# Kernel tuning notes

Hardware: AMD Instinct MI355X
Metric: run time of the kernel (lower is better)

Reference implementation:

```python
import jax, jax.numpy as jnp
import numpy as np

B, T, INP, OUT, H = 64, 512, 256, 256, 512


def _uniform(key, shape, scale):
    return jax.random.uniform(key, shape, jnp.float32, -scale, scale)


def lstm_proj(x, w_ih, w_hh, b, w_hr):
    """Single-layer LSTM with projection (torch nn.LSTM proj_size semantics).
    x: [B,T,D], w_ih: [4H,D], w_hh: [4H,P], b: [4H] (b_ih+b_hh), w_hr: [P,H].
    Returns hidden sequence [B,T,P]. Gate order: i, f, g, o."""
    # Precompute input contribution for all timesteps: [T,B,4H]
    xg = jnp.einsum('btd,gd->tbg', x, w_ih) + b
    Bsz = x.shape[0]
    P, Hh = w_hr.shape
    h0 = jnp.zeros((Bsz, P), x.dtype)
    c0 = jnp.zeros((Bsz, Hh), x.dtype)

    def step(carry, xg_t):
        h, c = carry
        gates = xg_t + h @ w_hh.T          # [B,4H]
        i, f, g, o = jnp.split(gates, 4, axis=-1)
        c = jax.nn.sigmoid(f) * c + jax.nn.sigmoid(i) * jnp.tanh(g)
        h = (jax.nn.sigmoid(o) * jnp.tanh(c)) @ w_hr.T  # projected hidden [B,P]
        return (h, c), h

    _, hs = jax.lax.scan(step, (h0, c0), xg)
    return hs.transpose(1, 0, 2)  # [B,T,P]


def setup_inputs() -> dict:
    key = jax.random.key(0)
    ks = jax.random.split(key, 10)
    s = 1.0 / np.sqrt(H)
    inp = jax.random.normal(ks[0], (B, T, INP), jnp.float32)
    out = jax.random.normal(ks[1], (B, T, OUT), jnp.float32)
    # lstm: input INP -> hidden H, proj OUT
    w_ih1 = _uniform(ks[2], (4 * H, INP), s)
    w_hh1 = _uniform(ks[3], (4 * H, OUT), s)
    b1 = _uniform(ks[4], (4 * H,), s) * 2.0  # b_ih + b_hh combined
    w_hr1 = _uniform(ks[5], (OUT, H), s)
    # lstm_reverse: input OUT -> hidden H, proj INP
    w_ih2 = _uniform(ks[6], (4 * H, OUT), s)
    w_hh2 = _uniform(ks[7], (4 * H, INP), s)
    b2 = _uniform(ks[8], (4 * H,), s) * 2.0
    w_hr2 = _uniform(ks[9], (INP, H), s)
    return {"inp": inp, "out": out,
            "w_ih1": w_ih1, "w_hh1": w_hh1, "b1": b1, "w_hr1": w_hr1,
            "w_ih2": w_ih2, "w_hh2": w_hh2, "b2": b2, "w_hr2": w_hr2}


def reference(inp, out, w_ih1, w_hh1, b1, w_hr1, w_ih2, w_hh2, b2, w_hr2):
    out2 = lstm_proj(inp, w_ih1, w_hh1, b1, w_hr1)   # [B,T,OUT]
    inp2 = lstm_proj(out, w_ih2, w_hh2, b2, w_hr2)   # [B,T,INP]
    return (inp2, out2)
```

## Files before the change

### kernel.cpp

```cpp
#include <hip/hip_runtime.h>

constexpr int kB = 64, kT = 512, kD = 256, kH = 512, kG = 2048;
constexpr int kNB = 256, kNT = 256;

typedef __attribute__((ext_vector_type(8))) short bf16x8;
typedef __attribute__((ext_vector_type(4))) float f32x4;
typedef unsigned long long ull;
union U4 { unsigned u[4]; ull q[2]; bf16x8 v; };

__device__ __forceinline__ ushort f2bf(float x) {
    union { float f; unsigned u; } v; v.f = x;
    unsigned r = v.u + 0x7FFFu + ((v.u >> 16) & 1u);
    return (ushort)(r >> 16);
}
__device__ __forceinline__ unsigned pk2(float a, float b) {
    return (unsigned)f2bf(a) | ((unsigned)f2bf(b) << 16);
}
__device__ __forceinline__ float sigm(float x) { return 1.f / (1.f + __expf(-x)); }

#define AT_LOAD(p)     __hip_atomic_load((p), __ATOMIC_RELAXED, __HIP_MEMORY_SCOPE_AGENT)
#define AT_LOAD64(p)   __hip_atomic_load((p), __ATOMIC_RELAXED, __HIP_MEMORY_SCOPE_AGENT)
#define AT_STORE(p,v)  __hip_atomic_store((p), (v), __ATOMIC_RELAXED, __HIP_MEMORY_SCOPE_AGENT)
#define AT_ADD(p,v)    __hip_atomic_fetch_add((p), (v), __ATOMIC_RELAXED, __HIP_MEMORY_SCOPE_AGENT)
#define VMCNT0() asm volatile("s_waitcnt vmcnt(0)" ::: "memory")

__global__ void bar_init_kernel(unsigned* ws) {
    int i = blockIdx.x * 1024 + threadIdx.x;
    if (i < 66560) AT_STORE(ws + i, 0u);
}

__global__ void __launch_bounds__(kNT, 1) lstm2_kernel(
    const float* __restrict__ x1, const float* __restrict__ x2,
    const float* __restrict__ wih1, const float* __restrict__ whh1,
    const float* __restrict__ b1,   const float* __restrict__ whr1,
    const float* __restrict__ wih2, const float* __restrict__ whh2,
    const float* __restrict__ b2,   const float* __restrict__ whr2,
    float* __restrict__ out, unsigned* __restrict__ ws)
{
    const int bid = blockIdx.x, tid = threadIdx.x;
    const int l = bid >> 7, b7 = bid & 127;
    const int bteam = b7 >> 5, blkh = b7 & 31;
    const int h0 = blkh * 16, grow0 = bteam * 16;
    const int l4bt = l * 4 + bteam;

    const float* x   = l ? x2 : x1;
    const float* wih = l ? wih2 : wih1;
    const float* whh = l ? whh2 : whh1;
    const float* bb  = l ? b2 : b1;
    const float* whr = l ? whr2 : whr1;
    float* outp = out + (l ? (size_t)0 : (size_t)kB * kT * kD);

    unsigned* TG  = ws + 256;
    unsigned* SDB = ws + 1024;
    unsigned* WC  = ws + 66560;

    __shared__ unsigned sst[16 * 268];
    __shared__ float lgs[4][16][17];

    {
        const int j  = b7 * 16 + (tid >> 4);
        const int k0 = (tid & 15) * 32;
        const float* whh_r = whh + (size_t)j * kD;
        float acc[32];
        #pragma unroll
        for (int i = 0; i < 32; i++) acc[i] = 0.f;
        for (int p = 0; p < kD; p++) {
            float w = whh_r[p];
            const float4* wr = (const float4*)(whr + (size_t)p * kH + k0);
            #pragma unroll
            for (int q = 0; q < 8; q++) {
                float4 v = wr[q];
                acc[q*4+0] = fmaf(w, v.x, acc[q*4+0]);
                acc[q*4+1] = fmaf(w, v.y, acc[q*4+1]);
                acc[q*4+2] = fmaf(w, v.z, acc[q*4+2]);
                acc[q*4+3] = fmaf(w, v.w, acc[q*4+3]);
            }
        }
        unsigned* dst = WC + (size_t)l * kG * 256 + (size_t)j * 256 + k0 / 2;
        #pragma unroll
        for (int i = 0; i < 16; i++) AT_STORE(dst + i, pk2(acc[2*i], acc[2*i+1]));
    }
    VMCNT0();
    __syncthreads();
    if (tid == 0) {
        unsigned a = AT_ADD(ws + 0, 1u);
        if (a == (unsigned)(kNB - 1)) AT_STORE(ws + 64, 1u);
        while (AT_LOAD(ws + 64) == 0u) __builtin_amdgcn_s_sleep(2);
    }
    __syncthreads();

    const int wv = tid >> 6, lane = tid & 63;
    const int n = lane & 15, kq = lane >> 4;
    const int gcol = wv * kH + h0 + n;
    const float bias = bb[gcol];
    const int mrow = grow0 + n;
    const int crow = tid >> 4, ccol = tid & 15;

    bf16x8 bxh[8];
    #pragma unroll
    for (int ks = 0; ks < 8; ks++) {
        const float4* p = (const float4*)(wih + (size_t)gcol * kD + ks * 32 + kq * 8);
        float4 a0 = p[0], a1 = p[1];
        U4 h;
        h.u[0] = pk2(a0.x, a0.y); h.u[1] = pk2(a0.z, a0.w);
        h.u[2] = pk2(a1.x, a1.y); h.u[3] = pk2(a1.z, a1.w);
        bxh[ks] = h.v;
    }
    bf16x8 bsh[16];
    {
        const ull* wcp = (const ull*)(WC + (size_t)l * kG * 256 + (size_t)gcol * 256);
        #pragma unroll
        for (int ks = 0; ks < 16; ks++) {
            U4 u;
            u.q[0] = AT_LOAD64(wcp + ks * 8 + kq * 2 + 0);
            u.q[1] = AT_LOAD64(wcp + ks * 8 + kq * 2 + 1);
            bsh[ks] = u.v;
        }
    }
    const bool isProj = (blkh < 16);
    bf16x8 bp[16];
    if (isProj) {
        const int pcol = blkh * 16 + n;
        #pragma unroll
        for (int ks = 0; ks < 16; ks++) {
            const float4* p = (const float4*)(whr + (size_t)pcol * kH + ks * 32 + kq * 8);
            float4 a0 = p[0], a1 = p[1];
            U4 h;
            h.u[0] = pk2(a0.x, a0.y); h.u[1] = pk2(a0.z, a0.w);
            h.u[2] = pk2(a1.x, a1.y); h.u[3] = pk2(a1.z, a1.w);
            bp[ks] = h.v;
        }
    }

    bf16x8 ax[8];
    #pragma unroll
    for (int ks = 0; ks < 8; ks++) {
        const float4* xp = (const float4*)(x + (size_t)mrow * kT * kD + ks * 32 + kq * 8);
        float4 a0 = xp[0], a1 = xp[1];
        U4 f;
        f.u[0] = pk2(a0.x, a0.y); f.u[1] = pk2(a0.z, a0.w);
        f.u[2] = pk2(a1.x, a1.y); f.u[3] = pk2(a1.z, a1.w);
        ax[ks] = f.v;
    }
    float creg = 0.f;

    const int srow = tid >> 4, scol = (tid & 15) * 16;

    for (int t = 0; t <= kT; ++t) {
        if (t == kT && !isProj) break;
        const int par = (t + 1) & 1;
        const unsigned want = (unsigned)t;
        const unsigned* tagp = TG + (l4bt * 2 + par) * 32;
        while (true) {
            unsigned tg = (lane < 32) ? AT_LOAD(tagp + lane) : want;
            if (__all((int)(tg >= want))) break;
            __builtin_amdgcn_s_sleep(1);
        }
        __builtin_amdgcn_sched_barrier(0);

        {
            const ull* sp = (const ull*)(SDB + (size_t)(l4bt * 2 + par) * 4096
                                             + srow * 256 + scol);
            ull* ld = (ull*)&sst[srow * 268 + scol];
            ull q0 = AT_LOAD64(sp + 0), q1 = AT_LOAD64(sp + 1);
            ull q2 = AT_LOAD64(sp + 2), q3 = AT_LOAD64(sp + 3);
            ull q4 = AT_LOAD64(sp + 4), q5 = AT_LOAD64(sp + 5);
            ull q6 = AT_LOAD64(sp + 6), q7 = AT_LOAD64(sp + 7);
            ld[0] = q0; ld[1] = q1; ld[2] = q2; ld[3] = q3;
            ld[4] = q4; ld[5] = q5; ld[6] = q6; ld[7] = q7;
        }
        __syncthreads();
        bf16x8 as[16];
        #pragma unroll
        for (int ks = 0; ks < 16; ks++)
            as[ks] = *(const bf16x8*)&sst[n * 268 + ks * 16 + kq * 4];

        if (t < kT) {
            f32x4 c0 = {bias, bias, bias, bias};
            f32x4 c1 = {0.f, 0.f, 0.f, 0.f};
            f32x4 c2 = {0.f, 0.f, 0.f, 0.f};
            #pragma unroll
            for (int ks = 0; ks < 8; ks++) {
                c0 = __builtin_amdgcn_mfma_f32_16x16x32_bf16(ax[ks],   bxh[ks],   c0, 0, 0, 0);
                c1 = __builtin_amdgcn_mfma_f32_16x16x32_bf16(as[ks],   bsh[ks],   c1, 0, 0, 0);
                c2 = __builtin_amdgcn_mfma_f32_16x16x32_bf16(as[8+ks], bsh[8+ks], c2, 0, 0, 0);
            }
            #pragma unroll
            for (int r = 0; r < 4; r++)
                lgs[wv][kq * 4 + r][n] = c0[r] + c1[r] + c2[r];
            __syncthreads();
            const float gi = sigm(lgs[0][crow][ccol]);
            const float gf = sigm(lgs[1][crow][ccol]);
            const float gg = tanhf(lgs[2][crow][ccol]);
            const float go = sigm(lgs[3][crow][ccol]);
            creg = gf * creg + gi * gg;
            const float sv = go * tanhf(creg);
            ushort* sd = (ushort*)(SDB + (size_t)(l4bt * 2 + (t & 1)) * 4096);
            __hip_atomic_store(sd + crow * 512 + h0 + ccol, f2bf(sv),
                               __ATOMIC_RELAXED, __HIP_MEMORY_SCOPE_AGENT);
            VMCNT0();
            __syncthreads();
            if (tid == 0)
                AT_STORE(TG + (l4bt * 2 + (t & 1)) * 32 + blkh, (unsigned)(t + 1));
        }

        if (t >= 1 && isProj) {
            f32x4 p0 = {0.f, 0.f, 0.f, 0.f};
            f32x4 p1 = {0.f, 0.f, 0.f, 0.f};
            #pragma unroll
            for (int ks = 0; ks < 8; ks++) {
                p0 = __builtin_amdgcn_mfma_f32_16x16x32_bf16(as[ks],     bp[ks],     p0, 0, 0, 0);
                p1 = __builtin_amdgcn_mfma_f32_16x16x32_bf16(as[8 + ks], bp[8 + ks], p1, 0, 0, 0);
            }
            const int pcol = blkh * 16 + n;
            #pragma unroll
            for (int r = 0; r < 4; r++)
                outp[((size_t)(grow0 + kq * 4 + r) * kT + (t - 1)) * kD + pcol] = p0[r] + p1[r];
        }

        if (t + 1 < kT) {
            #pragma unroll
            for (int ks = 0; ks < 8; ks++) {
                const float4* xp = (const float4*)(x + ((size_t)mrow * kT + (t + 1)) * kD + ks * 32 + kq * 8);
                float4 a0 = xp[0], a1 = xp[1];
                U4 f;
                f.u[0] = pk2(a0.x, a0.y); f.u[1] = pk2(a0.z, a0.w);
                f.u[2] = pk2(a1.x, a1.y); f.u[3] = pk2(a1.z, a1.w);
                ax[ks] = f.v;
            }
        }
    }
}

extern "C" void kernel_launch(void* const* d_in, const int* in_sizes, int n_in,
                              void* d_out, int out_size, void* d_ws, size_t ws_size,
                              hipStream_t stream) {
    const float* x1   = (const float*)d_in[0];
    const float* x2   = (const float*)d_in[1];
    const float* wih1 = (const float*)d_in[2];
    const float* whh1 = (const float*)d_in[3];
    const float* b1   = (const float*)d_in[4];
    const float* whr1 = (const float*)d_in[5];
    const float* wih2 = (const float*)d_in[6];
    const float* whh2 = (const float*)d_in[7];
    const float* b2   = (const float*)d_in[8];
    const float* whr2 = (const float*)d_in[9];
    float* outp  = (float*)d_out;
    unsigned* ws = (unsigned*)d_ws;

    bar_init_kernel<<<65, 1024, 0, stream>>>(ws);
    lstm2_kernel<<<dim3(kNB), dim3(kNT), 0, stream>>>(
        x1, x2, wih1, whh1, b1, whr1, wih2, whh2, b2, whr2, outp, ws);
}
```

Before: 3.067 ms.

## Map teams to blocks sharing an XCC and use non-atomic fast-path sync loads

Block-to-team mapping becomes interleaved (team = bid & 7), so each of the 8 recurrent teams is likely to sit on a single XCD. At runtime each block reads its XCC ID, and if all 32 blocks of a team share one XCC it switches the per-step tag polling and state exchange from agent-scope atomics to plain stores and sc0 loads. The aim is to cut inter-block synchronisation latency on every timestep. The workspace clearing moves into the kernel behind an extra grid barrier, and correctness relies on L2 coherence within an XCC and on the assumed block placement holding.

```diff
diff --git a/kernel.cpp b/kernel.cpp
--- a/kernel.cpp
+++ b/kernel.cpp
@@ -24,9 +24,44 @@
 #define AT_ADD(p,v)    __hip_atomic_fetch_add((p), (v), __ATOMIC_RELAXED, __HIP_MEMORY_SCOPE_AGENT)
 #define VMCNT0() asm volatile("s_waitcnt vmcnt(0)" ::: "memory")
 
+__device__ __forceinline__ unsigned ld_dw(const unsigned* p, bool fast) {
+    unsigned r;
+    if (fast) asm volatile("global_load_dword %0, %1, off sc0\n\ts_waitcnt vmcnt(0)"
+                           : "=v"(r) : "v"(p) : "memory");
+    else r = AT_LOAD(p);
+    return r;
+}
+__device__ __forceinline__ void ld8q(const ull* p, ull* q, bool fast) {
+    if (fast) {
+        asm volatile(
+            "global_load_dwordx2 %0, %8, off sc0\n\t"
+            "global_load_dwordx2 %1, %8, off offset:8 sc0\n\t"
+            "global_load_dwordx2 %2, %8, off offset:16 sc0\n\t"
+            "global_load_dwordx2 %3, %8, off offset:24 sc0\n\t"
+            "global_load_dwordx2 %4, %8, off offset:32 sc0\n\t"
+            "global_load_dwordx2 %5, %8, off offset:40 sc0\n\t"
+            "global_load_dwordx2 %6, %8, off offset:48 sc0\n\t"
+            "global_load_dwordx2 %7, %8, off offset:56 sc0\n\t"
+            "s_waitcnt vmcnt(0)"
+            : "=v"(q[0]), "=v"(q[1]), "=v"(q[2]), "=v"(q[3]),
+              "=v"(q[4]), "=v"(q[5]), "=v"(q[6]), "=v"(q[7])
+            : "v"(p) : "memory");
+    } else {
+        #pragma unroll
+        for (int i = 0; i < 8; i++) q[i] = AT_LOAD64(p + i);
+    }
+}
+__device__ __forceinline__ void st_u16(ushort* p, ushort v, bool fast) {
+    if (fast) *p = v;
+    else __hip_atomic_store(p, v, __ATOMIC_RELAXED, __HIP_MEMORY_SCOPE_AGENT);
+}
+__device__ __forceinline__ void st_dw(unsigned* p, unsigned v, bool fast) {
+    if (fast) *p = v;
+    else AT_STORE(p, v);
+}
+
 __global__ void bar_init_kernel(unsigned* ws) {
-    int i = blockIdx.x * 1024 + threadIdx.x;
-    if (i < 66560) AT_STORE(ws + i, 0u);
+    AT_STORE(ws + threadIdx.x, 0u);
 }
 
 __global__ void __launch_bounds__(kNT, 1) lstm2_kernel(
@@ -38,10 +73,9 @@
     float* __restrict__ out, unsigned* __restrict__ ws)
 {
     const int bid = blockIdx.x, tid = threadIdx.x;
-    const int l = bid >> 7, b7 = bid & 127;
-    const int bteam = b7 >> 5, blkh = b7 & 31;
+    const int team = bid & 7, rank = bid >> 3;
+    const int l = team >> 2, bteam = team & 3, blkh = rank;
     const int h0 = blkh * 16, grow0 = bteam * 16;
-    const int l4bt = l * 4 + bteam;
 
     const float* x   = l ? x2 : x1;
     const float* wih = l ? wih2 : wih1;
@@ -51,14 +85,24 @@
     float* outp = out + (l ? (size_t)0 : (size_t)kB * kT * kD);
 
     unsigned* TG  = ws + 256;
+    unsigned* XC  = ws + 768;
     unsigned* SDB = ws + 1024;
     unsigned* WC  = ws + 66560;
 
     __shared__ unsigned sst[16 * 268];
     __shared__ float lgs[4][16][17];
 
+    __builtin_amdgcn_fence(__ATOMIC_SEQ_CST, "agent");
+    VMCNT0();
+
+    unsigned xcc;
+    asm volatile("s_getreg_b32 %0, hwreg(HW_REG_XCC_ID)" : "=s"(xcc));
+    xcc &= 15u;
+    if (tid == 0) AT_STORE(XC + bid, xcc);
+
     {
-        const int j  = b7 * 16 + (tid >> 4);
+        const int wlin = bteam * 32 + rank;
+        const int j  = wlin * 16 + (tid >> 4);
         const int k0 = (tid & 15) * 32;
         const float* whh_r = whh + (size_t)j * kD;
         float acc[32];
@@ -89,7 +133,18 @@
     }
     __syncthreads();
 
-    const int wv = tid >> 6, lane = tid & 63;
+    const int lane = tid & 63;
+    unsigned x0 = AT_LOAD(XC + team);
+    unsigned xr = (lane < 32) ? AT_LOAD(XC + team + 8 * lane) : x0;
+    const bool fast = __all((int)(xr == x0));
+
+    if (rank == 0 && tid < 64) st_dw(TG + team * 64 + tid, 0u, fast);
+    if (tid < 128) {
+        st_dw(SDB + (size_t)(team * 2 + 0) * 4096 + rank * 128 + tid, 0u, fast);
+        st_dw(SDB + (size_t)(team * 2 + 1) * 4096 + rank * 128 + tid, 0u, fast);
+    }
+
+    const int wv = tid >> 6;
     const int n = lane & 15, kq = lane >> 4;
     const int gcol = wv * kH + h0 + n;
     const float bias = bb[gcol];
@@ -131,7 +186,6 @@
             bp[ks] = h.v;
         }
     }
-
     bf16x8 ax[8];
     #pragma unroll
     for (int ks = 0; ks < 8; ks++) {
@@ -143,31 +197,38 @@
         ax[ks] = f.v;
     }
     float creg = 0.f;
-
     const int srow = tid >> 4, scol = (tid & 15) * 16;
+
+    VMCNT0();
+    __syncthreads();
+    if (tid == 0) {
+        unsigned a = AT_ADD(ws + 128, 1u);
+        if (a == (unsigned)(kNB - 1)) AT_STORE(ws + 192, 1u);
+        while (AT_LOAD(ws + 192) == 0u) __builtin_amdgcn_s_sleep(2);
+    }
+    __syncthreads();
 
     for (int t = 0; t <= kT; ++t) {
         if (t == kT && !isProj) break;
         const int par = (t + 1) & 1;
         const unsigned want = (unsigned)t;
-        const unsigned* tagp = TG + (l4bt * 2 + par) * 32;
+        const unsigned* tagp = TG + (team * 2 + par) * 32;
         while (true) {
-            unsigned tg = (lane < 32) ? AT_LOAD(tagp + lane) : want;
+            unsigned tg = want;
+            if (lane < 32) tg = ld_dw(tagp + lane, fast);
             if (__all((int)(tg >= want))) break;
             __builtin_amdgcn_s_sleep(1);
         }
         __builtin_amdgcn_sched_barrier(0);
 
         {
-            const ull* sp = (const ull*)(SDB + (size_t)(l4bt * 2 + par) * 4096
+            const ull* sp = (const ull*)(SDB + (size_t)(team * 2 + par) * 4096
                                              + srow * 256 + scol);
+            ull q[8];
+            ld8q(sp, q, fast);
             ull* ld = (ull*)&sst[srow * 268 + scol];
-            ull q0 = AT_LOAD64(sp + 0), q1 = AT_LOAD64(sp + 1);
-            ull q2 = AT_LOAD64(sp + 2), q3 = AT_LOAD64(sp + 3);
-            ull q4 = AT_LOAD64(sp + 4), q5 = AT_LOAD64(sp + 5);
-            ull q6 = AT_LOAD64(sp + 6), q7 = AT_LOAD64(sp + 7);
-            ld[0] = q0; ld[1] = q1; ld[2] = q2; ld[3] = q3;
-            ld[4] = q4; ld[5] = q5; ld[6] = q6; ld[7] = q7;
+            #pragma unroll
+            for (int i = 0; i < 8; i++) ld[i] = q[i];
         }
         __syncthreads();
         bf16x8 as[16];
@@ -195,13 +256,12 @@
             const float go = sigm(lgs[3][crow][ccol]);
             creg = gf * creg + gi * gg;
             const float sv = go * tanhf(creg);
-            ushort* sd = (ushort*)(SDB + (size_t)(l4bt * 2 + (t & 1)) * 4096);
-            __hip_atomic_store(sd + crow * 512 + h0 + ccol, f2bf(sv),
-                               __ATOMIC_RELAXED, __HIP_MEMORY_SCOPE_AGENT);
+            ushort* sd = (ushort*)(SDB + (size_t)(team * 2 + (t & 1)) * 4096);
+            st_u16(sd + crow * 512 + h0 + ccol, f2bf(sv), fast);
             VMCNT0();
             __syncthreads();
             if (tid == 0)
-                AT_STORE(TG + (l4bt * 2 + (t & 1)) * 32 + blkh, (unsigned)(t + 1));
+                st_dw(TG + (team * 2 + (t & 1)) * 32 + rank, (unsigned)(t + 1), fast);
         }
 
         if (t >= 1 && isProj) {
@@ -248,7 +308,7 @@
     float* outp  = (float*)d_out;
     unsigned* ws = (unsigned*)d_ws;
 
-    bar_init_kernel<<<65, 1024, 0, stream>>>(ws);
+    bar_init_kernel<<<1, 1024, 0, stream>>>(ws);
     lstm2_kernel<<<dim3(kNB), dim3(kNT), 0, stream>>>(
         x1, x2, wih1, whh1, b1, whr1, wih2, whh2, b2, whr2, outp, ws);
 }
```

After: 2.957 ms. 3.6% less time.
